# Optimization experiments

Hardware: AMD Instinct MI355X
Metric: run time of the kernel (lower is better)

The kernel has to match this reference:

```python
import jax, jax.numpy as jnp
import numpy as np
import math

E = 39      # num_experts
D = 16      # STATE_DIM / d_model
DFF = 64    # d_ff
B = 32768   # batch of VM states (original runs one at a time)
OPCODE = 6  # slot of opcode in state vector
EPS = 1e-5  # torch LayerNorm default eps


def layernorm(x):
    # elementwise_affine=False LayerNorm over last dim, biased variance
    m = jnp.mean(x, axis=-1, keepdims=True)
    v = jnp.mean((x - m) ** 2, axis=-1, keepdims=True)
    return (x - m) / jnp.sqrt(v + EPS)


def setup_inputs() -> dict:
    key = jax.random.key(0)
    ks = jax.random.split(key, 10)
    state = jax.random.normal(ks[0], (B, D), dtype=jnp.float32)
    # opcode slot holds an integer-valued opcode in [0, E) so gating is realistic
    opcode = jax.random.randint(ks[1], (B,), 0, E).astype(jnp.float32)
    state = state.at[:, OPCODE].set(opcode)
    s = 0.1
    Wq = jax.random.normal(ks[2], (E, D, D), dtype=jnp.float32) * s
    Wk = jax.random.normal(ks[3], (E, D, D), dtype=jnp.float32) * s
    Wv = jax.random.normal(ks[4], (E, D, D), dtype=jnp.float32) * s
    Wo = jax.random.normal(ks[5], (E, D, D), dtype=jnp.float32) * s
    W1 = jax.random.normal(ks[6], (E, DFF, D), dtype=jnp.float32) * s
    b1 = jax.random.normal(ks[7], (E, DFF), dtype=jnp.float32) * s
    W2 = jax.random.normal(ks[8], (E, D, DFF), dtype=jnp.float32) * s
    b2 = jax.random.normal(ks[9], (E, D), dtype=jnp.float32) * s
    return {"state": state, "Wq": Wq, "Wk": Wk, "Wv": Wv, "Wo": Wo,
            "W1": W1, "b1": b1, "W2": W2, "b2": b2}


def reference(state, Wq, Wk, Wv, Wo, W1, b1, W2, b2):
    # --- OpcodeRouter: soft top-hat gates from the opcode slot ---
    opcode = state[:, OPCODE]                                  # [B]
    idx = jnp.arange(E, dtype=state.dtype)                     # [E]
    diff = opcode[:, None] - idx[None, :]                      # [B,E]
    gates = jax.nn.sigmoid((diff + 0.5) * 20.0) * jax.nn.sigmoid((-diff + 0.5) * 20.0)

    # --- All E experts on all B states, batched (x: seq_len == 1 token) ---
    xn = layernorm(state)                                      # [B,D]
    Q = jnp.einsum('bd,eod->beo', xn, Wq)                      # [B,E,D]
    K = jnp.einsum('bd,eod->beo', xn, Wk)
    V = jnp.einsum('bd,eod->beo', xn, Wv)
    scores = jnp.sum(Q * K, axis=-1, keepdims=True) / math.sqrt(D)  # [B,E,1]
    w = jax.nn.softmax(scores, axis=-1)                        # ones (seq_len 1), kept faithful
    attn = jnp.einsum('bev,ejv->bej', w * V, Wo)               # [B,E,D]
    x1 = state[:, None, :] + attn                              # residual 1

    xn2 = layernorm(x1)
    h = jax.nn.silu(jnp.einsum('bed,efd->bef', xn2, W1) + b1)  # [B,E,DFF]
    ffn = jnp.einsum('bef,edf->bed', h, W2) + b2               # [B,E,D]
    x2 = x1 + ffn                                              # residual 2

    # --- gated mixture of expert outputs ---
    return jnp.einsum('be,bed->bd', gates, x2)                 # [B,D]
```

## Files before the change

kernel.cpp:

```cpp
#include <hip/hip_runtime.h>
#include <math.h>

#define NE 39
#define ND 16
#define NB 32768
#define OPC 6
#define EPS 1e-5f
#define CAP 1280
#define TPE (CAP / 16)
#define NTILE (NE * TPE)
#define CHUNK 2
#define NCHUNK (NTILE / CHUNK)
#define CPE (TPE / CHUNK)

#define WVO_OFF 256
#define LIST_OFF (WVO_OFF + NE * 256 * 4)
#define WS_NEED (LIST_OFF + NE * CAP * 4)

#define GATE0 0.9999092022104184f

typedef __attribute__((ext_vector_type(8))) short bf16x8;
typedef __attribute__((ext_vector_type(4))) float f32x4;

__device__ __forceinline__ short bfr(float f) {
    unsigned u = __float_as_uint(f);
    u = (u + 0x7FFFu + ((u >> 16) & 1u)) >> 16;
    return (short)u;
}

__device__ __forceinline__ bf16x8 dupfrag(float a, float b, float c, float d) {
    const short s0 = bfr(a), s1 = bfr(b), s2 = bfr(c), s3 = bfr(d);
    bf16x8 r;
    r[0] = s0; r[1] = s1; r[2] = s2; r[3] = s3;
    r[4] = s0; r[5] = s1; r[6] = s2; r[7] = s3;
    return r;
}
__device__ __forceinline__ bf16x8 dupfragW(float4 v) {
    return dupfrag(0.5f * v.x, 0.5f * v.y, 0.5f * v.z, 0.5f * v.w);
}

__device__ __forceinline__ float siluf_(float a) {
    return a / (1.0f + __expf(-a));
}

__global__ __launch_bounds__(256) void k_scatter(const float* __restrict__ state,
                                                 const float* __restrict__ Wv,
                                                 const float* __restrict__ Wo,
                                                 int* __restrict__ cur,
                                                 float* __restrict__ wvo,
                                                 int* __restrict__ list) {
    __shared__ int lcnt[NE];
    __shared__ int lbase[NE];
    const int tid = threadIdx.x;
    const int bid = blockIdx.x;

    if (tid < NE) lcnt[tid] = 0;
    __syncthreads();
    const int r = bid * 256 + tid;
    const int e = (int)state[r * ND + OPC];
    const int rank = atomicAdd(&lcnt[e], 1);
    __syncthreads();
    if (tid < NE) lbase[tid] = (lcnt[tid] > 0) ? atomicAdd(&cur[tid], lcnt[tid]) : 0;
    __syncthreads();
    list[e * CAP + lbase[e] + rank] = r;

    if (bid < NE) {
        const int j = tid >> 4, d = tid & 15;
        const float* woRow = Wo + bid * 256 + j * 16;
        const float* wvCol = Wv + bid * 256 + d;
        float a = 0.0f;
        #pragma unroll
        for (int v = 0; v < 16; ++v) a += woRow[v] * wvCol[v * 16];
        wvo[bid * 256 + j * 16 + d] = a;
    }
}

__global__ __launch_bounds__(256, 2) void k_main(const float* __restrict__ state,
                                                 const int* __restrict__ cur,
                                                 const int* __restrict__ list,
                                                 const float* __restrict__ wvo,
                                                 const float* __restrict__ W1,
                                                 const float* __restrict__ b1,
                                                 const float* __restrict__ W2,
                                                 const float* __restrict__ b2,
                                                 float* __restrict__ out) {
    const int w = blockIdx.x * 4 + (threadIdx.x >> 6);
    if (w >= NCHUNK) return;
    const int lane = threadIdx.x & 63;
    const int g = lane >> 4;
    const int r16 = lane & 15;

    const int e = __builtin_amdgcn_readfirstlane(w / CPE);
    const int cnt = cur[e];
    const int base0 = (w * CHUNK - e * TPE) * 16;
    if (base0 >= cnt) return;

    const bf16x8 wvoF = dupfragW(*(const float4*)(wvo + e * 256 + r16 * 16 + 4 * g));
    bf16x8 w1F[4], w2F[4];
    float4 b1q[4];
    #pragma unroll
    for (int c = 0; c < 4; ++c) {
        w1F[c] = dupfragW(*(const float4*)(W1 + e * 1024 + (16 * c + r16) * 16 + 4 * g));
        w2F[c] = dupfragW(*(const float4*)(W2 + e * 1024 + r16 * 64 + 16 * c + 4 * g));
        b1q[c] = *(const float4*)(b1 + e * 64 + 16 * c + 4 * g);
    }
    const float4 b2q = *(const float4*)(b2 + e * 16 + 4 * g);
    const f32x4 z = {0.0f, 0.0f, 0.0f, 0.0f};

    auto tile = [&](int base) {
        const int slot = base + r16;
        const bool valid = slot < cnt;
        const int row = list[e * CAP + (valid ? slot : base)];

        const float4 x4 = *(const float4*)(state + row * 16 + 4 * g);

        float s = x4.x + x4.y + x4.z + x4.w;
        float q = x4.x * x4.x + x4.y * x4.y + x4.z * x4.z + x4.w * x4.w;
        s += __shfl_xor(s, 16); q += __shfl_xor(q, 16);
        s += __shfl_xor(s, 32); q += __shfl_xor(q, 32);
        const float m1 = s * 0.0625f;
        const float rs1 = rsqrtf(fmaxf(q * 0.0625f - m1 * m1, 0.0f) + EPS);
        const bf16x8 xnf = dupfrag((x4.x - m1) * rs1, (x4.y - m1) * rs1,
                                   (x4.z - m1) * rs1, (x4.w - m1) * rs1);

        const f32x4 at = __builtin_amdgcn_mfma_f32_16x16x32_bf16(wvoF, xnf, z, 0, 0, 0);

        const float x10 = x4.x + at[0], x11 = x4.y + at[1];
        const float x12 = x4.z + at[2], x13 = x4.w + at[3];
        float s2 = x10 + x11 + x12 + x13;
        float q2 = x10 * x10 + x11 * x11 + x12 * x12 + x13 * x13;
        s2 += __shfl_xor(s2, 16); q2 += __shfl_xor(q2, 16);
        s2 += __shfl_xor(s2, 32); q2 += __shfl_xor(q2, 32);
        const float m2 = s2 * 0.0625f;
        const float rs2 = rsqrtf(fmaxf(q2 * 0.0625f - m2 * m2, 0.0f) + EPS);
        const bf16x8 xn2f = dupfrag((x10 - m2) * rs2, (x11 - m2) * rs2,
                                    (x12 - m2) * rs2, (x13 - m2) * rs2);

        f32x4 ffn = z;
        #pragma unroll
        for (int c = 0; c < 4; ++c) {
            const f32x4 hc = __builtin_amdgcn_mfma_f32_16x16x32_bf16(w1F[c], xn2f, z, 0, 0, 0);
            const bf16x8 hfrag = dupfrag(siluf_(hc[0] + b1q[c].x),
                                         siluf_(hc[1] + b1q[c].y),
                                         siluf_(hc[2] + b1q[c].z),
                                         siluf_(hc[3] + b1q[c].w));
            ffn = __builtin_amdgcn_mfma_f32_16x16x32_bf16(w2F[c], hfrag, ffn, 0, 0, 0);
        }

        if (valid) {
            const float4 o4 = make_float4(GATE0 * (x10 + ffn[0] + b2q.x),
                                          GATE0 * (x11 + ffn[1] + b2q.y),
                                          GATE0 * (x12 + ffn[2] + b2q.z),
                                          GATE0 * (x13 + ffn[3] + b2q.w));
            *(float4*)(out + row * 16 + 4 * g) = o4;
        }
    };

    tile(base0);
    if (base0 + 16 < cnt) tile(base0 + 16);
}

__device__ __forceinline__ float dot16g(const float* __restrict__ w, const float* v) {
    float a0 = 0.f, a1 = 0.f, a2 = 0.f, a3 = 0.f;
    #pragma unroll
    for (int i = 0; i < 16; i += 4) {
        a0 += w[i+0] * v[i+0];
        a1 += w[i+1] * v[i+1];
        a2 += w[i+2] * v[i+2];
        a3 += w[i+3] * v[i+3];
    }
    return (a0 + a1) + (a2 + a3);
}

__global__ __launch_bounds__(64) void k_fallback(const float* __restrict__ state,
                                                 const float* __restrict__ Wv,
                                                 const float* __restrict__ Wo,
                                                 const float* __restrict__ W1,
                                                 const float* __restrict__ b1,
                                                 const float* __restrict__ W2,
                                                 const float* __restrict__ b2,
                                                 float* __restrict__ out) {
    const int row = blockIdx.x * 64 + threadIdx.x;
    const int e = (int)state[row * ND + OPC];

    float x[16];
    #pragma unroll
    for (int i = 0; i < 16; ++i) x[i] = state[row * 16 + i];

    float s = 0.f;
    #pragma unroll
    for (int i = 0; i < 16; ++i) s += x[i];
    const float m1 = s / 16.f;
    float v1 = 0.f;
    #pragma unroll
    for (int i = 0; i < 16; ++i) { const float d = x[i] - m1; v1 += d * d; }
    const float rs1 = rsqrtf(v1 / 16.f + EPS);
    float xn[16];
    #pragma unroll
    for (int i = 0; i < 16; ++i) xn[i] = (x[i] - m1) * rs1;

    float V[16];
    #pragma unroll
    for (int o = 0; o < 16; ++o) V[o] = dot16g(Wv + e * 256 + o * 16, xn);
    float x1[16];
    #pragma unroll
    for (int o = 0; o < 16; ++o) x1[o] = x[o] + dot16g(Wo + e * 256 + o * 16, V);

    float s2 = 0.f;
    #pragma unroll
    for (int i = 0; i < 16; ++i) s2 += x1[i];
    const float m2 = s2 / 16.f;
    float v2 = 0.f;
    #pragma unroll
    for (int i = 0; i < 16; ++i) { const float d = x1[i] - m2; v2 += d * d; }
    const float rs2 = rsqrtf(v2 / 16.f + EPS);
    float xn2[16];
    #pragma unroll
    for (int i = 0; i < 16; ++i) xn2[i] = (x1[i] - m2) * rs2;

    float r[16];
    #pragma unroll
    for (int o = 0; o < 16; ++o) r[o] = x1[o] + b2[e * 16 + o];

    #pragma unroll
    for (int c = 0; c < 4; ++c) {
        float hc[16];
        #pragma unroll
        for (int k = 0; k < 16; ++k) {
            const int f = c * 16 + k;
            const float a = b1[e * 64 + f] + dot16g(W1 + e * 1024 + f * 16, xn2);
            hc[k] = a / (1.0f + __expf(-a));
        }
        #pragma unroll
        for (int o = 0; o < 16; ++o)
            r[o] += dot16g(W2 + e * 1024 + o * 64 + c * 16, hc);
    }

    #pragma unroll
    for (int o = 0; o < 16; ++o) out[row * 16 + o] = GATE0 * r[o];
}

extern "C" void kernel_launch(void* const* d_in, const int* in_sizes, int n_in,
                              void* d_out, int out_size, void* d_ws, size_t ws_size,
                              hipStream_t stream) {
    const float* state = (const float*)d_in[0];
    const float* Wv = (const float*)d_in[3];
    const float* Wo = (const float*)d_in[4];
    const float* W1 = (const float*)d_in[5];
    const float* b1 = (const float*)d_in[6];
    const float* W2 = (const float*)d_in[7];
    const float* b2 = (const float*)d_in[8];
    float* out = (float*)d_out;

    if (ws_size >= (size_t)WS_NEED) {
        int* cur = (int*)d_ws;
        float* wvo = (float*)((char*)d_ws + WVO_OFF);
        int* list = (int*)((char*)d_ws + LIST_OFF);
        hipMemsetAsync(cur, 0, 256, stream);
        k_scatter<<<NB / 256, 256, 0, stream>>>(state, Wv, Wo, cur, wvo, list);
        k_main<<<(NCHUNK + 3) / 4, 256, 0, stream>>>(state, cur, list, wvo,
                                                     W1, b1, W2, b2, out);
    } else {
        k_fallback<<<NB / 64, 64, 0, stream>>>(state, Wv, Wo, W1, b1, W2, b2, out);
    }
}
```

Measured before the change: 20.72 us.

## Scatter state rows into expert-contiguous buffer and use one tile per wave

The scatter kernel now reads each full 16-float state row and writes it, along with its row id, into an expert-sorted contiguous buffer. The main kernel then reads inputs with coalesced loads instead of gathering through the index list. Per-expert counters are padded to separate cache lines to reduce atomic contention. Each wave now handles one 16-row tile instead of two, which doubles the wave count but also repeats the per-wave weight fragment loads. The cost is an extra global write and read of the whole state array in the scatter pass.

```diff
diff --git a/kernel.cpp b/kernel.cpp
--- a/kernel.cpp
+++ b/kernel.cpp
@@ -9,13 +9,12 @@
 #define CAP 1280
 #define TPE (CAP / 16)
 #define NTILE (NE * TPE)
-#define CHUNK 2
-#define NCHUNK (NTILE / CHUNK)
-#define CPE (TPE / CHUNK)
-
-#define WVO_OFF 256
-#define LIST_OFF (WVO_OFF + NE * 256 * 4)
-#define WS_NEED (LIST_OFF + NE * CAP * 4)
+
+#define CUR_OFF   0
+#define WVO_OFF   2560
+#define RID_OFF   (WVO_OFF + NE * 256 * 4)
+#define XBUF_OFF  (RID_OFF + NE * CAP * 4)
+#define WS_NEED   (XBUF_OFF + NE * CAP * 64)
 
 #define GATE0 0.9999092022104184f
 
@@ -48,7 +47,8 @@
                                                  const float* __restrict__ Wo,
                                                  int* __restrict__ cur,
                                                  float* __restrict__ wvo,
-                                                 int* __restrict__ list) {
+                                                 int* __restrict__ rowid,
+                                                 float4* __restrict__ xbuf) {
     __shared__ int lcnt[NE];
     __shared__ int lbase[NE];
     const int tid = threadIdx.x;
@@ -56,13 +56,22 @@
 
     if (tid < NE) lcnt[tid] = 0;
     __syncthreads();
+
     const int r = bid * 256 + tid;
-    const int e = (int)state[r * ND + OPC];
+    const float4* xs = (const float4*)(state + r * ND);
+    const float4 q0 = xs[0], q1 = xs[1], q2 = xs[2], q3 = xs[3];
+    const int e = (int)q1.z;
     const int rank = atomicAdd(&lcnt[e], 1);
     __syncthreads();
-    if (tid < NE) lbase[tid] = (lcnt[tid] > 0) ? atomicAdd(&cur[tid], lcnt[tid]) : 0;
+    if (tid < NE) lbase[tid] = (lcnt[tid] > 0) ? atomicAdd(&cur[tid * 16], lcnt[tid]) : 0;
     __syncthreads();
-    list[e * CAP + lbase[e] + rank] = r;
+
+    const int idx = e * CAP + lbase[e] + rank;
+    rowid[idx] = r;
+    xbuf[idx * 4 + 0] = q0;
+    xbuf[idx * 4 + 1] = q1;
+    xbuf[idx * 4 + 2] = q2;
+    xbuf[idx * 4 + 3] = q3;
 
     if (bid < NE) {
         const int j = tid >> 4, d = tid & 15;
@@ -75,9 +84,9 @@
     }
 }
 
-__global__ __launch_bounds__(256, 2) void k_main(const float* __restrict__ state,
-                                                 const int* __restrict__ cur,
-                                                 const int* __restrict__ list,
+__global__ __launch_bounds__(256, 2) void k_main(const int* __restrict__ cur,
+                                                 const int* __restrict__ rowid,
+                                                 const float4* __restrict__ xbuf,
                                                  const float* __restrict__ wvo,
                                                  const float* __restrict__ W1,
                                                  const float* __restrict__ b1,
@@ -85,15 +94,20 @@
                                                  const float* __restrict__ b2,
                                                  float* __restrict__ out) {
     const int w = blockIdx.x * 4 + (threadIdx.x >> 6);
-    if (w >= NCHUNK) return;
+    if (w >= NTILE) return;
     const int lane = threadIdx.x & 63;
     const int g = lane >> 4;
     const int r16 = lane & 15;
 
-    const int e = __builtin_amdgcn_readfirstlane(w / CPE);
-    const int cnt = cur[e];
-    const int base0 = (w * CHUNK - e * TPE) * 16;
-    if (base0 >= cnt) return;
+    const int e = __builtin_amdgcn_readfirstlane(w / TPE);
+    const int cnt = cur[e * 16];
+    const int base = (w - e * TPE) * 16;
+    if (base >= cnt) return;
+
+    const int idx = e * CAP + base + r16;
+    const float4 x4 = xbuf[idx * 4 + g];
+    const int row = rowid[idx];
+    const bool valid = (base + r16) < cnt;
 
     const bf16x8 wvoF = dupfragW(*(const float4*)(wvo + e * 256 + r16 * 16 + 4 * g));
     bf16x8 w1F[4], w2F[4];
@@ -107,57 +121,46 @@
     const float4 b2q = *(const float4*)(b2 + e * 16 + 4 * g);
     const f32x4 z = {0.0f, 0.0f, 0.0f, 0.0f};
 
-    auto tile = [&](int base) {
-        const int slot = base + r16;
-        const bool valid = slot < cnt;
-        const int row = list[e * CAP + (valid ? slot : base)];
-
-        const float4 x4 = *(const float4*)(state + row * 16 + 4 * g);
-
-        float s = x4.x + x4.y + x4.z + x4.w;
-        float q = x4.x * x4.x + x4.y * x4.y + x4.z * x4.z + x4.w * x4.w;
-        s += __shfl_xor(s, 16); q += __shfl_xor(q, 16);
-        s += __shfl_xor(s, 32); q += __shfl_xor(q, 32);
-        const float m1 = s * 0.0625f;
-        const float rs1 = rsqrtf(fmaxf(q * 0.0625f - m1 * m1, 0.0f) + EPS);
-        const bf16x8 xnf = dupfrag((x4.x - m1) * rs1, (x4.y - m1) * rs1,
-                                   (x4.z - m1) * rs1, (x4.w - m1) * rs1);
-
-        const f32x4 at = __builtin_amdgcn_mfma_f32_16x16x32_bf16(wvoF, xnf, z, 0, 0, 0);
-
-        const float x10 = x4.x + at[0], x11 = x4.y + at[1];
-        const float x12 = x4.z + at[2], x13 = x4.w + at[3];
-        float s2 = x10 + x11 + x12 + x13;
-        float q2 = x10 * x10 + x11 * x11 + x12 * x12 + x13 * x13;
-        s2 += __shfl_xor(s2, 16); q2 += __shfl_xor(q2, 16);
-        s2 += __shfl_xor(s2, 32); q2 += __shfl_xor(q2, 32);
-        const float m2 = s2 * 0.0625f;
-        const float rs2 = rsqrtf(fmaxf(q2 * 0.0625f - m2 * m2, 0.0f) + EPS);
-        const bf16x8 xn2f = dupfrag((x10 - m2) * rs2, (x11 - m2) * rs2,
-                                    (x12 - m2) * rs2, (x13 - m2) * rs2);
-
-        f32x4 ffn = z;
-        #pragma unroll
-        for (int c = 0; c < 4; ++c) {
-            const f32x4 hc = __builtin_amdgcn_mfma_f32_16x16x32_bf16(w1F[c], xn2f, z, 0, 0, 0);
-            const bf16x8 hfrag = dupfrag(siluf_(hc[0] + b1q[c].x),
-                                         siluf_(hc[1] + b1q[c].y),
-                                         siluf_(hc[2] + b1q[c].z),
-                                         siluf_(hc[3] + b1q[c].w));
-            ffn = __builtin_amdgcn_mfma_f32_16x16x32_bf16(w2F[c], hfrag, ffn, 0, 0, 0);
-        }
-
-        if (valid) {
-            const float4 o4 = make_float4(GATE0 * (x10 + ffn[0] + b2q.x),
-                                          GATE0 * (x11 + ffn[1] + b2q.y),
-                                          GATE0 * (x12 + ffn[2] + b2q.z),
-                                          GATE0 * (x13 + ffn[3] + b2q.w));
-            *(float4*)(out + row * 16 + 4 * g) = o4;
-        }
-    };
-
-    tile(base0);
-    if (base0 + 16 < cnt) tile(base0 + 16);
+    float s = x4.x + x4.y + x4.z + x4.w;
+    float q = x4.x * x4.x + x4.y * x4.y + x4.z * x4.z + x4.w * x4.w;
+    s += __shfl_xor(s, 16); q += __shfl_xor(q, 16);
+    s += __shfl_xor(s, 32); q += __shfl_xor(q, 32);
+    const float m1 = s * 0.0625f;
+    const float rs1 = rsqrtf(fmaxf(q * 0.0625f - m1 * m1, 0.0f) + EPS);
+    const bf16x8 xnf = dupfrag((x4.x - m1) * rs1, (x4.y - m1) * rs1,
+                               (x4.z - m1) * rs1, (x4.w - m1) * rs1);
+
+    const f32x4 at = __builtin_amdgcn_mfma_f32_16x16x32_bf16(wvoF, xnf, z, 0, 0, 0);
+
+    const float x10 = x4.x + at[0], x11 = x4.y + at[1];
+    const float x12 = x4.z + at[2], x13 = x4.w + at[3];
+    float s2 = x10 + x11 + x12 + x13;
+    float q2 = x10 * x10 + x11 * x11 + x12 * x12 + x13 * x13;
+    s2 += __shfl_xor(s2, 16); q2 += __shfl_xor(q2, 16);
+    s2 += __shfl_xor(s2, 32); q2 += __shfl_xor(q2, 32);
+    const float m2 = s2 * 0.0625f;
+    const float rs2 = rsqrtf(fmaxf(q2 * 0.0625f - m2 * m2, 0.0f) + EPS);
+    const bf16x8 xn2f = dupfrag((x10 - m2) * rs2, (x11 - m2) * rs2,
+                                (x12 - m2) * rs2, (x13 - m2) * rs2);
+
+    f32x4 ffn = z;
+    #pragma unroll
+    for (int c = 0; c < 4; ++c) {
+        const f32x4 hc = __builtin_amdgcn_mfma_f32_16x16x32_bf16(w1F[c], xn2f, z, 0, 0, 0);
+        const bf16x8 hfrag = dupfrag(siluf_(hc[0] + b1q[c].x),
+                                     siluf_(hc[1] + b1q[c].y),
+                                     siluf_(hc[2] + b1q[c].z),
+                                     siluf_(hc[3] + b1q[c].w));
+        ffn = __builtin_amdgcn_mfma_f32_16x16x32_bf16(w2F[c], hfrag, ffn, 0, 0, 0);
+    }
+
+    if (valid) {
+        const float4 o4 = make_float4(GATE0 * (x10 + ffn[0] + b2q.x),
+                                      GATE0 * (x11 + ffn[1] + b2q.y),
+                                      GATE0 * (x12 + ffn[2] + b2q.z),
+                                      GATE0 * (x13 + ffn[3] + b2q.w));
+        *(float4*)(out + row * ND + 4 * g) = o4;
+    }
 }
 
 __device__ __forceinline__ float dot16g(const float* __restrict__ w, const float* v) {
@@ -253,13 +256,15 @@
     float* out = (float*)d_out;
 
     if (ws_size >= (size_t)WS_NEED) {
-        int* cur = (int*)d_ws;
-        float* wvo = (float*)((char*)d_ws + WVO_OFF);
-        int* list = (int*)((char*)d_ws + LIST_OFF);
-        hipMemsetAsync(cur, 0, 256, stream);
-        k_scatter<<<NB / 256, 256, 0, stream>>>(state, Wv, Wo, cur, wvo, list);
-        k_main<<<(NCHUNK + 3) / 4, 256, 0, stream>>>(state, cur, list, wvo,
-                                                     W1, b1, W2, b2, out);
+        int* cur      = (int*)((char*)d_ws + CUR_OFF);
+        float* wvo    = (float*)((char*)d_ws + WVO_OFF);
+        int* rowid    = (int*)((char*)d_ws + RID_OFF);
+        float4* xbuf  = (float4*)((char*)d_ws + XBUF_OFF);
+
+        hipMemsetAsync(cur, 0, 2560, stream);
+        k_scatter<<<NB / 256, 256, 0, stream>>>(state, Wv, Wo, cur, wvo, rowid, xbuf);
+        k_main<<<(NTILE + 3) / 4, 256, 0, stream>>>(cur, rowid, xbuf, wvo,
+                                                    W1, b1, W2, b2, out);
     } else {
         k_fallback<<<NB / 64, 64, 0, stream>>>(state, Wv, Wo, W1, b1, W2, b2, out);
     }
```

Measured after the change: 22.44 us. +8.3%, slower.
